# Optimization experiments

Measured on AMD Instinct MI355X. Metric: run time of the kernel, lower is better.

Reference implementation:

```python
import jax, jax.numpy as jnp
import numpy as np
from math import sqrt

B, L, H, D = 4, 4096, 8, 64
FACTOR = 5


def setup_inputs():
    key = jax.random.key(0)
    k1, k2, k3, k4 = jax.random.split(key, 4)
    queries = jax.random.normal(k1, (B, L, H, D), dtype=jnp.float32)
    keys = jax.random.normal(k2, (B, L, H, D), dtype=jnp.float32)
    values = jax.random.normal(k3, (B, L, H, D), dtype=jnp.float32)
    sample_k = min(FACTOR * int(np.ceil(np.log(L))), L)  # U_part = 45
    index_sample = jax.random.randint(k4, (L, sample_k), 0, L)
    return {"queries": queries, "keys": keys, "values": values,
            "index_sample": index_sample}


def reference(queries, keys, values, index_sample):
    Bq, L_Q, Hq, Dq = queries.shape
    L_K = keys.shape[1]
    Q = jnp.transpose(queries, (0, 2, 1, 3))  # [B,H,L_Q,D]
    K = jnp.transpose(keys, (0, 2, 1, 3))     # [B,H,L_K,D]
    V = jnp.transpose(values, (0, 2, 1, 3))   # [B,H,L_K,D]
    n_top = min(FACTOR * int(np.ceil(np.log(L_Q))), L_Q)  # u = 45

    # --- _prob_QK: randomly-sampled QK scoring + top-k query selection ---
    K_sample = K[:, :, index_sample, :]                       # [B,H,L_Q,sample_k,D]
    Q_K_sample = jnp.einsum('bhld,bhlkd->bhlk', Q, K_sample)  # [B,H,L_Q,sample_k]
    M = Q_K_sample.max(-1) - Q_K_sample.sum(-1) / L_K         # sparsity measure
    _, M_top = jax.lax.top_k(M, n_top)                        # [B,H,u] query indices
    Q_reduce = jnp.take_along_axis(Q, M_top[..., None], axis=2)  # [B,H,u,D]
    scores = jnp.einsum('bhud,bhkd->bhuk', Q_reduce, K)       # [B,H,u,L_K]

    # scale = 1/sqrt(D) (self.scale is None)
    scores = scores * (1.0 / sqrt(Dq))

    # --- ProbMask (mask_flag=True): causal, key j masked if j > query idx ---
    mask = jnp.arange(L_K)[None, None, None, :] > M_top[..., None]
    scores = jnp.where(mask, -jnp.inf, scores)
    attn = jax.nn.softmax(scores, axis=-1)                    # [B,H,u,L_K]

    # --- initial context (masked case): cumulative sum of V over time ---
    context = jnp.cumsum(V, axis=2)                           # [B,H,L_Q,D]

    # --- scatter attn@V into the selected query positions ---
    upd = jnp.einsum('bhuk,bhkd->bhud', attn, V)              # [B,H,u,D]
    b_idx = jnp.arange(Bq)[:, None, None]
    h_idx = jnp.arange(Hq)[None, :, None]
    context = context.at[b_idx, h_idx, M_top].set(upd)
    return context  # [B,H,L_Q,D], as returned by the torch module
```

## Files before the change

kernel.cpp:

```cpp
#include <hip/hip_runtime.h>

#define NB 4
#define LSEQ 4096
#define NH 8
#define ND 64
#define NSAMP 45
#define NTOP 45
#define ACH 256
#define NCH (LSEQ / ACH)
#define SENT 0x7fffffff

typedef float f32x4 __attribute__((ext_vector_type(4)));

__global__ __launch_bounds__(256) void prep_kernel(
        const int* __restrict__ idxS, int* __restrict__ sortedAB) {
    int t = threadIdx.x;
    int l = blockIdx.x * 256 + t;
    const int* is = idxS + (size_t)l * NSAMP;
    __shared__ int cnt[256][17];
    #pragma unroll
    for (int c = 0; c < 16; ++c) cnt[t][c] = 0;
    for (int s = 0; s < NSAMP; ++s) cnt[t][is[s] >> 8] += 1;
    int run = 0;
    #pragma unroll
    for (int c = 0; c < 16; ++c) { int v = cnt[t][c]; cnt[t][c] = run; run += v; }
    int* ab = sortedAB + (size_t)l * 48;
    ab[23] = SENT; ab[46] = SENT; ab[47] = SENT;
    for (int s = 0; s < NSAMP; ++s) {
        int idx = is[s];
        int p = cnt[t][idx >> 8]++;
        ab[(p & 1) * 24 + (p >> 1)] = (idx << 8) | s;
    }
}

__global__ __launch_bounds__(512, 4) void compute_M_kernel(
        const float* __restrict__ Q,
        const float* __restrict__ K,
        const int* __restrict__ sortedAB,
        float* __restrict__ Mout) {
    int xcd = blockIdx.x & 7;
    int sub = blockIdx.x >> 3;
    int bh  = (xcd << 2) | (sub & 3);
    int lt  = sub >> 2;
    int b = bh >> 3, h = bh & 7;
    int t = threadIdx.x;
    int lloc = t & 255;
    int par  = t >> 8;
    int l = (lt << 8) | lloc;

    __shared__ float Ks[256 * 68];
    __shared__ float redM[512];
    __shared__ float redS[512];

    f32x4 qa[16];
    {
        const f32x4* qp0 = reinterpret_cast<const f32x4*>(
            Q + (((size_t)b * LSEQ + l) * NH + h) * ND);
        #pragma unroll
        for (int i = 0; i < 16; ++i) qa[i] = __builtin_nontemporal_load(qp0 + i);
    }

    auto dotQK = [&](const f32x4 (&q4)[16], const float* kr) -> float {
        const f32x4* k4 = reinterpret_cast<const f32x4*>(kr);
        float w[32];
        #pragma unroll
        for (int i = 0; i < 8; ++i) {
            f32x4 a = q4[i], bb = k4[i], c = q4[i + 8], d4 = k4[i + 8];
            w[4 * i + 0] = __fadd_rn(__fmul_rn(a.x, bb.x), __fmul_rn(c.x, d4.x));
            w[4 * i + 1] = __fadd_rn(__fmul_rn(a.y, bb.y), __fmul_rn(c.y, d4.y));
            w[4 * i + 2] = __fadd_rn(__fmul_rn(a.z, bb.z), __fmul_rn(c.z, d4.z));
            w[4 * i + 3] = __fadd_rn(__fmul_rn(a.w, bb.w), __fmul_rn(c.w, d4.w));
        }
        #pragma unroll
        for (int off = 16; off; off >>= 1) {
            #pragma unroll
            for (int i = 0; i < off; ++i) w[i] = __fadd_rn(w[i], w[i + off]);
        }
        return w[0];
    };

    const int* sp = sortedAB + (size_t)l * 48 + par * 24;
    int ptr = 0;
    int pk = sp[0];

    size_t kbh = ((size_t)b * LSEQ * NH + h) * ND;

    float maxv = -INFINITY;
    float sumv = 0.0f;

    for (int c = 0; c < 16; ++c) {
        #pragma unroll
        for (int i = 0; i < 8; ++i) {
            int flat = i * 512 + t;
            int row = flat >> 4, col = flat & 15;
            f32x4 v = *reinterpret_cast<const f32x4*>(
                K + kbh + (size_t)(c * 256 + row) * (NH * ND) + col * 4);
            *reinterpret_cast<f32x4*>(&Ks[row * 68 + col * 4]) = v;
        }
        __syncthreads();

        while ((pk >> 16) == c) {
            int r = (pk >> 8) & 255;
            float p = dotQK(qa, &Ks[r * 68]);
            maxv = fmaxf(maxv, p);
            sumv = __fadd_rn(sumv, p);
            ++ptr;
            pk = sp[ptr];
        }
        __syncthreads();
    }

    redM[t] = maxv; redS[t] = sumv;
    __syncthreads();
    if (t < 256) {
        float m = fmaxf(redM[t], redM[t + 256]);
        float s = __fadd_rn(redS[t], redS[t + 256]);
        Mout[(size_t)bh * LSEQ + l] = m - s * (1.0f / (float)LSEQ);
    }
}

__global__ __launch_bounds__(256) void topk_kernel(
        const float* __restrict__ M, int* __restrict__ Mtop) {
    int bh = blockIdx.x;
    int t = threadIdx.x;
    int wave = t >> 6, lane = t & 63;
    const float* m = M + (size_t)bh * LSEQ;

    float rv[16];
    #pragma unroll
    for (int k = 0; k < 16; ++k) rv[k] = m[t + (k << 8)];

    __shared__ float wv[4];
    __shared__ int   wi[4];
    __shared__ int   winIdx;

    for (int iter = 0; iter < NTOP; ++iter) {
        float bv = -INFINITY; int bi = 0x7fffffff;
        #pragma unroll
        for (int k = 0; k < 16; ++k) {
            float v = rv[k];
            if (v > bv) { bv = v; bi = t + (k << 8); }
        }
        #pragma unroll
        for (int off = 1; off < 64; off <<= 1) {
            float ov = __shfl_xor(bv, off, 64);
            int   oi = __shfl_xor(bi, off, 64);
            if (ov > bv || (ov == bv && oi < bi)) { bv = ov; bi = oi; }
        }
        if (lane == 0) { wv[wave] = bv; wi[wave] = bi; }
        __syncthreads();
        if (t == 0) {
            float cv = wv[0]; int ci = wi[0];
            for (int ww = 1; ww < 4; ++ww) {
                if (wv[ww] > cv || (wv[ww] == cv && wi[ww] < ci)) { cv = wv[ww]; ci = wi[ww]; }
            }
            winIdx = ci;
            Mtop[bh * NTOP + iter] = ci;
        }
        __syncthreads();
        int widx = winIdx;
        #pragma unroll
        for (int k = 0; k < 16; ++k)
            if (widx == t + (k << 8)) rv[k] = -INFINITY;
        __syncthreads();
    }
}

__global__ __launch_bounds__(256) void cumsumA_kernel(
        const float* __restrict__ V, float* __restrict__ chunkSums) {
    int blk = blockIdx.x;
    int c = blk & 15;
    int bh = blk >> 4;
    int h = bh & (NH - 1);
    int b = bh >> 3;
    int g = threadIdx.x >> 6, d = threadIdx.x & 63;

    const size_t rstride = (size_t)NH * ND;
    size_t vbase = (size_t)b * LSEQ * rstride + (size_t)h * ND + d;

    int l0 = c * 256 + g * 64;
    float s = 0.0f;
    for (int l = l0; l < l0 + 64; ++l) s += V[vbase + (size_t)l * rstride];

    __shared__ float part[4][ND];
    part[g][d] = s;
    __syncthreads();
    if (threadIdx.x < ND)
        chunkSums[(size_t)blk * ND + d] =
            part[0][d] + part[1][d] + part[2][d] + part[3][d];
}

__global__ __launch_bounds__(256) void cumsumC_kernel(
        const float* __restrict__ V, const float* __restrict__ chunkSums,
        float* __restrict__ out) {
    int blk = blockIdx.x;
    int c = blk & 15;
    int bh = blk >> 4;
    int h = bh & (NH - 1);
    int b = bh >> 3;
    int g = threadIdx.x >> 6, d = threadIdx.x & 63;

    const size_t rstride = (size_t)NH * ND;
    size_t vbase = (size_t)b * LSEQ * rstride + (size_t)h * ND + d;

    float run = 0.0f;
    for (int cc = 0; cc < c; ++cc)
        run += chunkSums[((size_t)bh * 16 + cc) * ND + d];

    int l0 = c * 256 + g * 64;
    float s = 0.0f;
    for (int l = l0; l < l0 + 64; ++l) s += V[vbase + (size_t)l * rstride];
    __shared__ float part[4][ND];
    part[g][d] = s;
    __syncthreads();
    for (int gg = 0; gg < g; ++gg) run += part[gg][d];

    size_t obase = (size_t)bh * LSEQ * ND + d;
    for (int l = l0; l < l0 + 64; ++l) {
        run += V[vbase + (size_t)l * rstride];
        out[obase + (size_t)l * ND] = run;
    }
}

__global__ __launch_bounds__(256, 1) void attn_partial_kernel(
        const float* __restrict__ Q, const float* __restrict__ K,
        const float* __restrict__ V, const int* __restrict__ Mtop,
        float* __restrict__ part) {
    int bh = blockIdx.x >> 4;
    int c  = blockIdx.x & 15;
    int b = bh >> 3, h = bh & 7;
    int t = threadIdx.x;
    int w = t >> 6, lane = t & 63;
    int jj = lane >> 4, dq = lane & 15;

    __shared__ float Qs[NTOP * ND];
    __shared__ int   posS[NTOP];
    __shared__ float Vs[64][68];
    __shared__ float Pw[4][64];

    size_t base = ((size_t)b * LSEQ * NH + h) * ND;

    if (t < NTOP) posS[t] = Mtop[bh * NTOP + t];
    __syncthreads();
    for (int idx = t; idx < NTOP * 16; idx += 256) {
        int u = idx >> 4, cg = idx & 15;
        f32x4 v = *reinterpret_cast<const f32x4*>(
            Q + base + (size_t)posS[u] * (NH * ND) + cg * 4);
        *reinterpret_cast<f32x4*>(&Qs[u * ND + cg * 4]) = v;
    }

    f32x4 o[12];
    float mreg[12], sreg[12];
    #pragma unroll
    for (int qi = 0; qi < 12; ++qi) {
        o[qi] = 0.0f; mreg[qi] = -INFINITY; sreg[qi] = 0.0f;
    }

    for (int tt = 0; tt < ACH / 64; ++tt) {
        int tile0 = c * ACH + tt * 64;
        __syncthreads();
        #pragma unroll
        for (int i = 0; i < 4; ++i) {
            int flat = i * 256 + t;
            int r = flat >> 4, cg = flat & 15;
            f32x4 v = *reinterpret_cast<const f32x4*>(
                V + base + (size_t)(tile0 + r) * (NH * ND) + cg * 4);
            *reinterpret_cast<f32x4*>(&Vs[r][cg * 4]) = v;
        }
        __syncthreads();

        f32x4 kreg[16];
        #pragma unroll
        for (int i = 0; i < 16; ++i)
            kreg[i] = *reinterpret_cast<const f32x4*>(
                K + base + (size_t)(tile0 + lane) * (NH * ND) + i * 4);

        #pragma unroll
        for (int qi = 0; qi < 12; ++qi) {
            int u = w + 4 * qi;
            if (u >= NTOP) continue;
            int pu = posS[u];
            if (pu < tile0) continue;

            float a0 = 0, a1 = 0, a2 = 0, a3 = 0;
            #pragma unroll
            for (int di = 0; di < 16; ++di) {
                f32x4 qv = *reinterpret_cast<const f32x4*>(&Qs[u * ND + di * 4]);
                a0 = fmaf(qv.x, kreg[di].x, a0);
                a1 = fmaf(qv.y, kreg[di].y, a1);
                a2 = fmaf(qv.z, kreg[di].z, a2);
                a3 = fmaf(qv.w, kreg[di].w, a3);
            }
            float sc = ((a0 + a1) + (a2 + a3)) * 0.125f;
            if (tile0 + lane > pu) sc = -INFINITY;

            float tmax = sc;
            #pragma unroll
            for (int off = 1; off < 64; off <<= 1)
                tmax = fmaxf(tmax, __shfl_xor(tmax, off, 64));
            float mold = mreg[qi];
            float mnew = fmaxf(mold, tmax);
            float alpha = __expf(mold - mnew);
            float e = __expf(sc - mnew);
            float esum = e;
            #pragma unroll
            for (int off = 1; off < 64; off <<= 1)
                esum += __shfl_xor(esum, off, 64);
            sreg[qi] = sreg[qi] * alpha + esum;
            mreg[qi] = mnew;
            Pw[w][lane] = e;
            o[qi] *= alpha;
            #pragma unroll
            for (int i = 0; i < 16; ++i) {
                float pe = Pw[w][i * 4 + jj];
                f32x4 vv = *reinterpret_cast<const f32x4*>(&Vs[i * 4 + jj][dq * 4]);
                o[qi] += vv * pe;
            }
        }
    }

    #pragma unroll
    for (int qi = 0; qi < 12; ++qi) {
        int u = w + 4 * qi;
        if (u >= NTOP) continue;
        if (posS[u] < c * ACH) continue;
        f32x4 oo = o[qi];
        #pragma unroll
        for (int off = 16; off <= 32; off <<= 1) {
            oo.x += __shfl_xor(oo.x, off, 64);
            oo.y += __shfl_xor(oo.y, off, 64);
            oo.z += __shfl_xor(oo.z, off, 64);
            oo.w += __shfl_xor(oo.w, off, 64);
        }
        size_t pb = ((size_t)(bh * NTOP + u) * NCH + c) * 72;
        if (lane < 16)
            *reinterpret_cast<f32x4*>(&part[pb + 4 + dq * 4]) = oo;
        if (lane == 0) { part[pb] = mreg[qi]; part[pb + 1] = sreg[qi]; }
    }
}

__global__ __launch_bounds__(256) void attn_merge_kernel(
        const float* __restrict__ part, const int* __restrict__ Mtop,
        float* __restrict__ ctx) {
    int j = blockIdx.x * 4 + (threadIdx.x >> 6);
    int lane = threadIdx.x & 63;
    int bh = j / NTOP, u = j - bh * NTOP;
    int pos = Mtop[bh * NTOP + u];
    int cmax = pos >> 8;
    size_t pb0 = (size_t)(bh * NTOP + u) * NCH * 72;
    float m = -INFINITY;
    for (int cc = 0; cc <= cmax; ++cc)
        m = fmaxf(m, part[pb0 + (size_t)cc * 72]);
    float S = 0.0f, oacc = 0.0f;
    for (int cc = 0; cc <= cmax; ++cc) {
        float mc = part[pb0 + (size_t)cc * 72];
        float sc = part[pb0 + (size_t)cc * 72 + 1];
        float wgt = __expf(mc - m);
        S = fmaf(sc, wgt, S);
        oacc = fmaf(part[pb0 + (size_t)cc * 72 + 4 + lane], wgt, oacc);
    }
    ctx[(size_t)j * ND + lane] = oacc / S;
}

__global__ __launch_bounds__(256) void scatter_kernel(
        const float* __restrict__ ctx, const int* __restrict__ Mtop,
        float* __restrict__ out) {
    int j = blockIdx.x * 4 + (threadIdx.x >> 6);
    int lane = threadIdx.x & 63;
    int bh = j / NTOP, u = j - bh * NTOP;
    int pos = Mtop[bh * NTOP + u];
    out[((size_t)bh * LSEQ + pos) * ND + lane] = ctx[(size_t)j * ND + lane];
}

#define TJ 64
__global__ __launch_bounds__(256) void attn_rows_kernel(
        const float* __restrict__ Q,
        const float* __restrict__ K,
        const float* __restrict__ V,
        const int* __restrict__ Mtop,
        float* __restrict__ out) {
    int x = blockIdx.x;
    int xcd = x & 7;
    int slot = x >> 3;
    int grp = slot / NTOP;
    int u = slot % NTOP;
    int bh = grp * 8 + xcd;
    int h = bh & (NH - 1);
    int b = bh >> 3;
    int pos = Mtop[bh * NTOP + u];
    int n = pos + 1;
    int t = threadIdx.x;
    int r = t >> 2, qt = t & 3;

    __shared__ float Ks[TJ][65];
    __shared__ float Vs[TJ][65];
    __shared__ float red[256];

    const size_t rstride = (size_t)NH * ND;
    size_t base = (size_t)b * LSEQ * rstride + (size_t)h * ND;

    float qreg[16];
    const float* qrow = Q + base + (size_t)pos * rstride + qt * 16;
    #pragma unroll
    for (int i = 0; i < 16; i += 4) {
        float4 v4 = *reinterpret_cast<const float4*>(qrow + i);
        qreg[i] = v4.x; qreg[i + 1] = v4.y; qreg[i + 2] = v4.z; qreg[i + 3] = v4.w;
    }

    float m = -INFINITY, s = 0.0f;
    float o[16];
    #pragma unroll
    for (int dd = 0; dd < 16; ++dd) o[dd] = 0.0f;

    int ntiles = (n + TJ - 1) / TJ;
    for (int tt = 0; tt < ntiles; ++tt) {
        int j0 = tt * TJ;
        __syncthreads();
        #pragma unroll
        for (int i = 0; i < 4; ++i) {
            int u16 = t + i * 256;
            int rr = u16 >> 4, cc = u16 & 15;
            int j = j0 + rr;
            int jc = (j < n) ? j : (n - 1);
            const float* rowk = K + base + (size_t)jc * rstride;
            float4 kv = *reinterpret_cast<const float4*>(rowk + cc * 4);
            Ks[rr][cc * 4 + 0] = kv.x; Ks[rr][cc * 4 + 1] = kv.y;
            Ks[rr][cc * 4 + 2] = kv.z; Ks[rr][cc * 4 + 3] = kv.w;
            const float* rowv = V + base + (size_t)jc * rstride;
            float4 vv = *reinterpret_cast<const float4*>(rowv + cc * 4);
            Vs[rr][cc * 4 + 0] = vv.x; Vs[rr][cc * 4 + 1] = vv.y;
            Vs[rr][cc * 4 + 2] = vv.z; Vs[rr][cc * 4 + 3] = vv.w;
        }
        __syncthreads();

        int j = j0 + r;
        float acc = 0.0f;
        #pragma unroll
        for (int dd = 0; dd < 16; ++dd)
            acc = fmaf(qreg[dd], Ks[r][qt * 16 + dd], acc);
        acc += __shfl_xor(acc, 1, 64);
        acc += __shfl_xor(acc, 2, 64);

        if (j < n) {
            float sc = acc * 0.125f;
            if (sc > m) {
                float alpha = __expf(m - sc);
                s *= alpha;
                #pragma unroll
                for (int dd = 0; dd < 16; ++dd) o[dd] *= alpha;
                m = sc;
            }
            float e = __expf(sc - m);
            s += e;
            #pragma unroll
            for (int dd = 0; dd < 16; ++dd)
                o[dd] = fmaf(e, Vs[r][qt * 16 + dd], o[dd]);
        }
    }
    __syncthreads();

    red[t] = m; __syncthreads();
    for (int sft = 128; sft; sft >>= 1) {
        if (t < sft) red[t] = fmaxf(red[t], red[t + sft]);
        __syncthreads();
    }
    float mstar = red[0]; __syncthreads();
    float a = __expf(m - mstar);

    red[t] = s * a; __syncthreads();
    for (int sft = 128; sft; sft >>= 1) {
        if (t < sft) red[t] += red[t + sft];
        __syncthreads();
    }
    float S = red[0]; __syncthreads();

    float* OB = &Ks[0][0];
    #pragma unroll
    for (int dd = 0; dd < 16; ++dd) OB[t * 16 + dd] = o[dd] * a;
    __syncthreads();

    if (t < ND) {
        int qtt = t >> 4, dd = t & 15;
        float tot = 0.0f;
        for (int k = 0; k < 64; ++k) tot += OB[(4 * k + qtt) * 16 + dd];
        out[((size_t)bh * LSEQ + pos) * ND + t] = tot / S;
    }
}

extern "C" void kernel_launch(void* const* d_in, const int* in_sizes, int n_in,
                              void* d_out, int out_size, void* d_ws, size_t ws_size,
                              hipStream_t stream) {
    const float* Q = (const float*)d_in[0];
    const float* K = (const float*)d_in[1];
    const float* V = (const float*)d_in[2];
    const int* idxS = (const int*)d_in[3];
    float* out = (float*)d_out;

    float* Mbuf = (float*)d_out;
    int*   sortedAB = (int*)((char*)d_out + (1 << 20));
    float* part = (float*)((char*)d_out + (2 << 20));
    int*   Mtop = (int*)d_ws;
    float* chunkSums = (float*)((char*)d_ws + 8192);
    float* ctx = (float*)((char*)d_ws + 8192 + 131072);
    size_t wsNeeded = 8192 + 131072 + (size_t)NB * NH * NTOP * ND * 4;

    prep_kernel<<<LSEQ / 256, 256, 0, stream>>>(idxS, sortedAB);
    compute_M_kernel<<<512, 512, 0, stream>>>(Q, K, sortedAB, Mbuf);
    topk_kernel<<<NB * NH, 256, 0, stream>>>(Mbuf, Mtop);

    if (ws_size >= wsNeeded) {
        attn_partial_kernel<<<NB * NH * NCH, 256, 0, stream>>>(Q, K, V, Mtop, part);
        attn_merge_kernel<<<NB * NH * NTOP / 4, 256, 0, stream>>>(part, Mtop, ctx);
        cumsumA_kernel<<<NB * NH * 16, 256, 0, stream>>>(V, chunkSums);
        cumsumC_kernel<<<NB * NH * 16, 256, 0, stream>>>(V, chunkSums, out);
        scatter_kernel<<<NB * NH * NTOP / 4, 256, 0, stream>>>(ctx, Mtop, out);
    } else {
        cumsumA_kernel<<<NB * NH * 16, 256, 0, stream>>>(V, chunkSums);
        cumsumC_kernel<<<NB * NH * 16, 256, 0, stream>>>(V, chunkSums, out);
        attn_rows_kernel<<<NB * NH * NTOP, 256, 0, stream>>>(Q, K, V, Mtop, out);
    }
}
```

Baseline: 428.0 us.

## Transpose K tile in LDS and use 1024-thread blocks in compute_M

The compute_M kernel now stores each 256-row K chunk transposed in shared memory, with a padded stride of 257. It computes each sampled dot product with scalar FMAs into eight accumulators, replacing the vectorized row reads and tree reduction. Blocks grow to 1024 threads covering 512 queries each, halving the grid so each K chunk loaded into LDS serves twice as many queries. In exchange it issues four times as many scalar LDS reads and writes. The launch bound of 1024 threads with min 4 blocks may force register pressure and spills for the 64-float Q array.

```diff
diff --git a/kernel.cpp b/kernel.cpp
--- a/kernel.cpp
+++ b/kernel.cpp
@@ -9,6 +9,7 @@
 #define ACH 256
 #define NCH (LSEQ / ACH)
 #define SENT 0x7fffffff
+#define KSTRIDE 257
 
 typedef float f32x4 __attribute__((ext_vector_type(4)));
 
@@ -33,7 +34,7 @@
     }
 }
 
-__global__ __launch_bounds__(512, 4) void compute_M_kernel(
+__global__ __launch_bounds__(1024, 4) void compute_M_kernel(
         const float* __restrict__ Q,
         const float* __restrict__ K,
         const int* __restrict__ sortedAB,
@@ -44,40 +45,25 @@
     int lt  = sub >> 2;
     int b = bh >> 3, h = bh & 7;
     int t = threadIdx.x;
-    int lloc = t & 255;
-    int par  = t >> 8;
-    int l = (lt << 8) | lloc;
-
-    __shared__ float Ks[256 * 68];
-    __shared__ float redM[512];
-    __shared__ float redS[512];
-
-    f32x4 qa[16];
+    int lloc = t & 511;
+    int par  = t >> 9;
+    int l = (lt << 9) | lloc;
+
+    __shared__ float KsT[64 * KSTRIDE];
+    __shared__ float redM[1024];
+    __shared__ float redS[1024];
+
+    float qs[64];
     {
-        const f32x4* qp0 = reinterpret_cast<const f32x4*>(
+        const f32x4* qp = reinterpret_cast<const f32x4*>(
             Q + (((size_t)b * LSEQ + l) * NH + h) * ND);
         #pragma unroll
-        for (int i = 0; i < 16; ++i) qa[i] = __builtin_nontemporal_load(qp0 + i);
-    }
-
-    auto dotQK = [&](const f32x4 (&q4)[16], const float* kr) -> float {
-        const f32x4* k4 = reinterpret_cast<const f32x4*>(kr);
-        float w[32];
-        #pragma unroll
-        for (int i = 0; i < 8; ++i) {
-            f32x4 a = q4[i], bb = k4[i], c = q4[i + 8], d4 = k4[i + 8];
-            w[4 * i + 0] = __fadd_rn(__fmul_rn(a.x, bb.x), __fmul_rn(c.x, d4.x));
-            w[4 * i + 1] = __fadd_rn(__fmul_rn(a.y, bb.y), __fmul_rn(c.y, d4.y));
-            w[4 * i + 2] = __fadd_rn(__fmul_rn(a.z, bb.z), __fmul_rn(c.z, d4.z));
-            w[4 * i + 3] = __fadd_rn(__fmul_rn(a.w, bb.w), __fmul_rn(c.w, d4.w));
-        }
-        #pragma unroll
-        for (int off = 16; off; off >>= 1) {
-            #pragma unroll
-            for (int i = 0; i < off; ++i) w[i] = __fadd_rn(w[i], w[i + off]);
-        }
-        return w[0];
-    };
+        for (int i = 0; i < 16; ++i) {
+            f32x4 v = __builtin_nontemporal_load(qp + i);
+            qs[4 * i + 0] = v.x; qs[4 * i + 1] = v.y;
+            qs[4 * i + 2] = v.z; qs[4 * i + 3] = v.w;
+        }
+    }
 
     const int* sp = sortedAB + (size_t)l * 48 + par * 24;
     int ptr = 0;
@@ -90,18 +76,37 @@
 
     for (int c = 0; c < 16; ++c) {
         #pragma unroll
-        for (int i = 0; i < 8; ++i) {
-            int flat = i * 512 + t;
-            int row = flat >> 4, col = flat & 15;
+        for (int i = 0; i < 4; ++i) {
+            int flat = i * 1024 + t;
+            int row = flat >> 4, cg = flat & 15;
             f32x4 v = *reinterpret_cast<const f32x4*>(
-                K + kbh + (size_t)(c * 256 + row) * (NH * ND) + col * 4);
-            *reinterpret_cast<f32x4*>(&Ks[row * 68 + col * 4]) = v;
+                K + kbh + (size_t)(c * 256 + row) * (NH * ND) + cg * 4);
+            KsT[(4 * cg + 0) * KSTRIDE + row] = v.x;
+            KsT[(4 * cg + 1) * KSTRIDE + row] = v.y;
+            KsT[(4 * cg + 2) * KSTRIDE + row] = v.z;
+            KsT[(4 * cg + 3) * KSTRIDE + row] = v.w;
         }
         __syncthreads();
 
         while ((pk >> 16) == c) {
             int r = (pk >> 8) & 255;
-            float p = dotQK(qa, &Ks[r * 68]);
+            const float* kcol = &KsT[r];
+            float acc0 = 0.f, acc1 = 0.f, acc2 = 0.f, acc3 = 0.f;
+            float acc4 = 0.f, acc5 = 0.f, acc6 = 0.f, acc7 = 0.f;
+            #pragma unroll
+            for (int d = 0; d < 64; d += 8) {
+                acc0 = fmaf(qs[d + 0], kcol[(d + 0) * KSTRIDE], acc0);
+                acc1 = fmaf(qs[d + 1], kcol[(d + 1) * KSTRIDE], acc1);
+                acc2 = fmaf(qs[d + 2], kcol[(d + 2) * KSTRIDE], acc2);
+                acc3 = fmaf(qs[d + 3], kcol[(d + 3) * KSTRIDE], acc3);
+                acc4 = fmaf(qs[d + 4], kcol[(d + 4) * KSTRIDE], acc4);
+                acc5 = fmaf(qs[d + 5], kcol[(d + 5) * KSTRIDE], acc5);
+                acc6 = fmaf(qs[d + 6], kcol[(d + 6) * KSTRIDE], acc6);
+                acc7 = fmaf(qs[d + 7], kcol[(d + 7) * KSTRIDE], acc7);
+            }
+            float p = __fadd_rn(
+                __fadd_rn(__fadd_rn(acc0, acc4), __fadd_rn(acc2, acc6)),
+                __fadd_rn(__fadd_rn(acc1, acc5), __fadd_rn(acc3, acc7)));
             maxv = fmaxf(maxv, p);
             sumv = __fadd_rn(sumv, p);
             ++ptr;
@@ -112,9 +117,9 @@
 
     redM[t] = maxv; redS[t] = sumv;
     __syncthreads();
-    if (t < 256) {
-        float m = fmaxf(redM[t], redM[t + 256]);
-        float s = __fadd_rn(redS[t], redS[t + 256]);
+    if (t < 512) {
+        float m = fmaxf(redM[t], redM[t + 512]);
+        float s = __fadd_rn(redS[t], redS[t + 512]);
         Mout[(size_t)bh * LSEQ + l] = m - s * (1.0f / (float)LSEQ);
     }
 }
@@ -505,7 +510,7 @@
     size_t wsNeeded = 8192 + 131072 + (size_t)NB * NH * NTOP * ND * 4;
 
     prep_kernel<<<LSEQ / 256, 256, 0, stream>>>(idxS, sortedAB);
-    compute_M_kernel<<<512, 512, 0, stream>>>(Q, K, sortedAB, Mbuf);
+    compute_M_kernel<<<256, 1024, 0, stream>>>(Q, K, sortedAB, Mbuf);
     topk_kernel<<<NB * NH, 256, 0, stream>>>(Mbuf, Mtop);
 
     if (ws_size >= wsNeeded) {
```

New measurement: 472.8 us. 1.1x slower.
